# Optimization experiments

Hardware: AMD Instinct MI355X
Metric: run time of the kernel (lower is better)

## Reference

```python
import jax, jax.numpy as jnp
import numpy as np

B, S, D_MODEL = 8, 1024, 1024
N_HEADS, N_KV_HEADS, HEAD_DIM = 16, 8, 64
ROPE_THETA = 10000.0
LN_EPS = 1e-12


def setup_inputs() -> dict:
    key = jax.random.key(0)
    ks = jax.random.split(key, 6)
    sc = 0.02
    return {
        "hidden_states": jax.random.normal(ks[0], (B, S, D_MODEL), jnp.float32),
        "Wq": jax.random.normal(ks[1], (D_MODEL, N_HEADS * HEAD_DIM), jnp.float32) * sc,
        "bq": jnp.zeros((N_HEADS * HEAD_DIM,), jnp.float32),
        "Wk": jax.random.normal(ks[2], (D_MODEL, N_KV_HEADS * HEAD_DIM), jnp.float32) * sc,
        "bk": jnp.zeros((N_KV_HEADS * HEAD_DIM,), jnp.float32),
        "Wv": jax.random.normal(ks[3], (D_MODEL, N_KV_HEADS * HEAD_DIM), jnp.float32) * sc,
        "bv": jnp.zeros((N_KV_HEADS * HEAD_DIM,), jnp.float32),
        "Wo": jax.random.normal(ks[4], (N_HEADS * HEAD_DIM, D_MODEL), jnp.float32) * sc,
        "bo": jnp.zeros((D_MODEL,), jnp.float32),
        "ln_gamma": jnp.ones((D_MODEL,), jnp.float32),
        "ln_beta": jnp.zeros((D_MODEL,), jnp.float32),
    }


def _rope_tables(seq_len, dim, dtype):
    # lucidrains RotaryEmbedding: inv_freq over even indices, interleaved pairs
    inv_freq = 1.0 / (ROPE_THETA ** (jnp.arange(0, dim, 2, dtype=jnp.float32) / dim))
    angles = jnp.arange(seq_len, dtype=jnp.float32)[:, None] * inv_freq[None, :]  # [S, dim/2]
    return jnp.cos(angles).astype(dtype), jnp.sin(angles).astype(dtype)


def _apply_rope(x, cos, sin):
    # x: [B, S, H, D]; rotate interleaved pairs (x0,x1),(x2,x3),...
    x1 = x[..., 0::2]
    x2 = x[..., 1::2]
    c = cos[None, :, None, :]
    s = sin[None, :, None, :]
    y1 = x1 * c - x2 * s
    y2 = x1 * s + x2 * c
    return jnp.stack([y1, y2], axis=-1).reshape(x.shape)


def reference(hidden_states, Wq, bq, Wk, bk, Wv, bv, Wo, bo, ln_gamma, ln_beta):
    b, s, _ = hidden_states.shape
    q = (hidden_states @ Wq + bq).reshape(b, s, N_HEADS, HEAD_DIM)
    k = (hidden_states @ Wk + bk).reshape(b, s, N_KV_HEADS, HEAD_DIM)
    v = (hidden_states @ Wv + bv).reshape(b, s, N_KV_HEADS, HEAD_DIM)

    cos, sin = _rope_tables(s, HEAD_DIM, hidden_states.dtype)
    q = _apply_rope(q, cos, sin)
    k = _apply_rope(k, cos, sin)

    # GQA: repeat_interleave kv heads to match query heads (factor 2)
    rep = N_HEADS // N_KV_HEADS
    k = jnp.repeat(k, rep, axis=2)  # [B, S, H, D]
    v = jnp.repeat(v, rep, axis=2)

    scale = 1.0 / jnp.sqrt(jnp.asarray(HEAD_DIM, hidden_states.dtype))
    scores = jnp.einsum('bqhd,bkhd->bhqk', q * scale, k)  # [B, H, S, S]
    probs = jax.nn.softmax(scores, axis=-1)
    attn = jnp.einsum('bhqk,bkhd->bqhd', probs, v).reshape(b, s, N_HEADS * HEAD_DIM)

    out = attn @ Wo + bo
    resid = out + hidden_states
    mu = jnp.mean(resid, axis=-1, keepdims=True)
    var = jnp.mean(jnp.square(resid - mu), axis=-1, keepdims=True)
    normed = (resid - mu) * jax.lax.rsqrt(var + LN_EPS)
    return normed * ln_gamma + ln_beta
```

## Files before the change

kernel.cpp:

```cpp
#include <hip/hip_runtime.h>
#include <math.h>
#include <stdint.h>

typedef unsigned short u16;
typedef __bf16 bf16x8 __attribute__((ext_vector_type(8)));
typedef float f32x4 __attribute__((ext_vector_type(4)));

typedef const __attribute__((address_space(1))) void gv_t;
typedef __attribute__((address_space(3))) void lv_t;

__device__ __forceinline__ u16 f2bf(float f) {
    unsigned u = __builtin_bit_cast(unsigned, f);
    return (u16)((u + 0x7FFFu + ((u >> 16) & 1u)) >> 16);
}
__device__ __forceinline__ float bf2f(u16 h) {
    return __builtin_bit_cast(float, (unsigned)h << 16);
}
__device__ __forceinline__ void gll16(const void* g, void* l) {
    __builtin_amdgcn_global_load_lds((gv_t*)(uintptr_t)g,
                                     (lv_t*)(unsigned)(uintptr_t)l, 16, 0, 0);
}

__global__ __launch_bounds__(256) void cvt_bf16_kernel(
    const float* __restrict__ in, u16* __restrict__ out, int n4)
{
    int i = blockIdx.x * 256 + threadIdx.x;
    if (i >= n4) return;
    float4 f = ((const float4*)in)[i];
    ushort4 o = make_ushort4(f2bf(f.x), f2bf(f.y), f2bf(f.z), f2bf(f.w));
    ((ushort4*)out)[i] = o;
}

__global__ __launch_bounds__(256) void cvt_t4_kernel(
    const float* __restrict__ w0, const float* __restrict__ w1,
    const float* __restrict__ w2, const float* __restrict__ w3,
    u16* __restrict__ o0, u16* __restrict__ o1,
    u16* __restrict__ o2, u16* __restrict__ o3)
{
    __shared__ u16 t[64][65];
    const float* in; u16* out; int N;
    switch (blockIdx.z) {
        case 0: in = w0; out = o0; N = 1024; break;
        case 1: in = w1; out = o1; N = 512;  break;
        case 2: in = w2; out = o2; N = 512;  break;
        default: in = w3; out = o3; N = 1024; break;
    }
    int kb = blockIdx.y * 64, nb = blockIdx.x * 64;
    if (nb >= N) return;
    int tid = threadIdx.x;
#pragma unroll
    for (int c = 0; c < 16; ++c) {
        int id = c * 256 + tid;
        int r = id >> 6, n = id & 63;
        t[n][r] = f2bf(in[(size_t)(kb + r) * N + nb + n]);
    }
    __syncthreads();
#pragma unroll
    for (int c = 0; c < 16; ++c) {
        int id = c * 256 + tid;
        int r = id >> 6, n = id & 63;
        out[(size_t)(nb + r) * 1024 + kb + n] = t[r][n];
    }
}

template<int MODE>
__global__ __launch_bounds__(256) void gemm_mfma(
    const u16* __restrict__ A, const u16* __restrict__ Bt,
    const float* __restrict__ b0, const float* __restrict__ b1,
    const float* __restrict__ b2,
    const float* __restrict__ resid, float* __restrict__ Cf,
    u16* __restrict__ Qo, u16* __restrict__ Ko, u16* __restrict__ Vto,
    int N, int K)
{
    __shared__ __align__(16) u16 Asl[128 * 64];
    __shared__ __align__(16) u16 Bsl[128 * 64];
    const int tid = threadIdx.x, lane = tid & 63, w = tid >> 6;
    const int quad = lane >> 4, l16 = lane & 15;
    const int bm = blockIdx.y * 128, bn = blockIdx.x * 128;
    const int wm = (w >> 1) * 64, wn = (w & 1) * 64;

    f32x4 acc[4][4] = {};

    const int dr = lane >> 3;
    const int dcs = (((lane & 7) ^ dr) << 3);
    const u16* Ag = &A[(size_t)(bm + w * 32 + dr) * K + dcs];
    const u16* Bg = &Bt[(size_t)(bn + w * 32 + dr) * K + dcs];
    u16* Al = &Asl[(w * 32) * 64];
    u16* Bl = &Bsl[(w * 32) * 64];

    const int sw = l16 & 7;

    for (int k0 = 0; k0 < K; k0 += 64) {
#pragma unroll
        for (int c = 0; c < 4; ++c) {
            gll16(Ag + (size_t)(c * 8) * K + k0, Al + c * 8 * 64);
            gll16(Bg + (size_t)(c * 8) * K + k0, Bl + c * 8 * 64);
        }
        __syncthreads();
        bf16x8 af[4][2], bfr[4][2];
#pragma unroll
        for (int i = 0; i < 4; ++i)
#pragma unroll
            for (int ks = 0; ks < 2; ++ks)
                af[i][ks] = *(const bf16x8*)&Asl[(wm + i * 16 + l16) * 64 + (((ks * 4 + quad) ^ sw) << 3)];
#pragma unroll
        for (int j = 0; j < 4; ++j)
#pragma unroll
            for (int ks = 0; ks < 2; ++ks)
                bfr[j][ks] = *(const bf16x8*)&Bsl[(wn + j * 16 + l16) * 64 + (((ks * 4 + quad) ^ sw) << 3)];
#pragma unroll
        for (int i = 0; i < 4; ++i)
#pragma unroll
            for (int j = 0; j < 4; ++j)
#pragma unroll
                for (int ks = 0; ks < 2; ++ks)
                    acc[i][j] = __builtin_amdgcn_mfma_f32_16x16x32_bf16(af[i][ks], bfr[j][ks], acc[i][j], 0, 0, 0);
        __syncthreads();
    }

#pragma unroll
    for (int j = 0; j < 4; ++j) {
        int col = bn + wn + j * 16 + l16;
        if (MODE == 1) {
            float bb = b0[col];
#pragma unroll
            for (int i = 0; i < 4; ++i) {
                int row0 = bm + wm + i * 16 + quad * 4;
#pragma unroll
                for (int r = 0; r < 4; ++r) {
                    size_t off = (size_t)(row0 + r) * N + col;
                    Cf[off] = acc[i][j][r] + bb + resid[off];
                }
            }
        } else if (col < 1024) {
            float bb = b0[col];
#pragma unroll
            for (int i = 0; i < 4; ++i) {
                int row0 = bm + wm + i * 16 + quad * 4;
#pragma unroll
                for (int r = 0; r < 4; ++r)
                    Qo[(size_t)(row0 + r) * 1024 + col] = f2bf(acc[i][j][r] + bb);
            }
        } else if (col < 1536) {
            int c2 = col - 1024;
            float bb = b1[c2];
#pragma unroll
            for (int i = 0; i < 4; ++i) {
                int row0 = bm + wm + i * 16 + quad * 4;
#pragma unroll
                for (int r = 0; r < 4; ++r)
                    Ko[(size_t)(row0 + r) * 512 + c2] = f2bf(acc[i][j][r] + bb);
            }
        } else {
            int c2 = col - 1536, kvh = c2 >> 6, d = c2 & 63;
            float bb = b2[c2];
#pragma unroll
            for (int i = 0; i < 4; ++i) {
                int row0 = bm + wm + i * 16 + quad * 4;
                int b = row0 >> 10, s = row0 & 1023;
                ushort4 o4;
                o4.x = f2bf(acc[i][j][0] + bb);
                o4.y = f2bf(acc[i][j][1] + bb);
                o4.z = f2bf(acc[i][j][2] + bb);
                o4.w = f2bf(acc[i][j][3] + bb);
                *(ushort4*)&Vto[(size_t)((b * 8 + kvh) * 64 + d) * 1024 + s] = o4;
            }
        }
    }
}

__global__ __launch_bounds__(256) void rope_bf16_kernel(
    u16* __restrict__ x, int shift, int stride, int total)
{
    int idx = blockIdx.x * 256 + threadIdx.x;
    if (idx >= total) return;
    int j = idx & 31;
    int h = (idx >> 5) & ((1 << shift) - 1);
    int row = idx >> (5 + shift);
    int pos = row & 1023;
    float inv = exp2f((float)j * -0.4152410118609203f);
    float sn, cs;
    sincosf((float)pos * inv, &sn, &cs);
    unsigned* p = (unsigned*)&x[(size_t)row * stride + h * 64 + (j << 1)];
    unsigned u = *p;
    float x1 = bf2f((u16)(u & 0xffff)), x2 = bf2f((u16)(u >> 16));
    float y1 = x1 * cs - x2 * sn, y2 = x1 * sn + x2 * cs;
    *p = (unsigned)f2bf(y1) | ((unsigned)f2bf(y2) << 16);
}

__global__ __launch_bounds__(256) void attn_mfma(
    const u16* __restrict__ Q, const u16* __restrict__ K,
    const u16* __restrict__ Vt, u16* __restrict__ O)
{
    __shared__ __align__(16) u16 Ks[64 * 64];
    __shared__ __align__(16) u16 Vts[64 * 64];
    __shared__ __align__(16) u16 Ps[128][40];

    const int tid = threadIdx.x, lane = tid & 63, w = tid >> 6;
    const int quad = lane >> 4, l16 = lane & 15;
    const int qt = blockIdx.x, h = blockIdx.y, b = blockIdx.z;
    const int kvh = h >> 1;
    const size_t qrow0 = (size_t)b * 1024 + qt * 128;
    const size_t krow0 = (size_t)b * 1024;
    const u16* Vg = Vt + (size_t)((b * 8 + kvh) * 64) * 1024;

    const int dr = lane >> 3;
    const int dcs = (((lane & 7) ^ dr) << 3);
    const u16* Kg0 = &K[(krow0 + w * 16 + dr) * 512 + kvh * 64 + dcs];
    const u16* Vg0 = &Vg[(size_t)(w * 16 + dr) * 1024 + dcs];
    u16* Kl0 = &Ks[(w * 16) * 64];
    u16* Vl0 = &Vts[(w * 16) * 64];
    const int sw = l16 & 7;

    bf16x8 qf[2][2];
#pragma unroll
    for (int qg = 0; qg < 2; ++qg) {
        int qrow = w * 32 + qg * 16 + l16;
        float fpos = (float)(qt * 128 + qrow);
#pragma unroll
        for (int ks = 0; ks < 2; ++ks) {
            uint4 qraw = *(const uint4*)&Q[(qrow0 + qrow) * 1024 + h * 64 + ks * 32 + quad * 8];
            unsigned o_[4];
#pragma unroll
            for (int t = 0; t < 4; ++t) {
                int j = ks * 16 + quad * 4 + t;
                float inv = exp2f((float)j * -0.4152410118609203f);
                float sn_, cs_;
                sincosf(fpos * inv, &sn_, &cs_);
                unsigned u = (&qraw.x)[t];
                float x1 = bf2f((u16)(u & 0xffff)), x2 = bf2f((u16)(u >> 16));
                float y1 = x1 * cs_ - x2 * sn_, y2 = x1 * sn_ + x2 * cs_;
                o_[t] = (unsigned)f2bf(y1) | ((unsigned)f2bf(y2) << 16);
            }
            qf[qg][ks] = __builtin_bit_cast(bf16x8, make_uint4(o_[0], o_[1], o_[2], o_[3]));
        }
    }

    f32x4 acc_o[2][4] = {};
    float l_i[2] = {0.f, 0.f};
    const float C1 = 0.18033688011112043f;

    for (int kt = 0; kt < 16; ++kt) {
#pragma unroll
        for (int c = 0; c < 2; ++c) {
            gll16(Kg0 + (size_t)(kt * 64 + c * 8) * 512, Kl0 + c * 8 * 64);
            gll16(Vg0 + (size_t)(c * 8) * 1024 + kt * 64, Vl0 + c * 8 * 64);
        }
        __syncthreads();

        f32x4 s[2][4] = {};
#pragma unroll
        for (int ks = 0; ks < 2; ++ks) {
#pragma unroll
            for (int nt = 0; nt < 4; ++nt) {
                bf16x8 ak = *(const bf16x8*)&Ks[(nt * 16 + l16) * 64 + (((ks * 4 + quad) ^ sw) << 3)];
                s[0][nt] = __builtin_amdgcn_mfma_f32_16x16x32_bf16(ak, qf[0][ks], s[0][nt], 0, 0, 0);
                s[1][nt] = __builtin_amdgcn_mfma_f32_16x16x32_bf16(ak, qf[1][ks], s[1][nt], 0, 0, 0);
            }
        }

#pragma unroll
        for (int kc = 0; kc < 2; ++kc) {
#pragma unroll
            for (int qg = 0; qg < 2; ++qg) {
                float sum = 0.f;
#pragma unroll
                for (int ntl = 0; ntl < 2; ++ntl) {
                    int nt = kc * 2 + ntl;
                    unsigned pk0, pk1;
                    {
                        float p0 = __builtin_amdgcn_exp2f(s[qg][nt][0] * C1);
                        float p1 = __builtin_amdgcn_exp2f(s[qg][nt][1] * C1);
                        unsigned u0 = __builtin_bit_cast(unsigned, p0);
                        unsigned u1 = __builtin_bit_cast(unsigned, p1);
                        sum += __builtin_bit_cast(float, u0 & 0xffff0000u);
                        sum += __builtin_bit_cast(float, u1 & 0xffff0000u);
                        pk0 = __builtin_amdgcn_perm(u1, u0, 0x07060302u);
                    }
                    {
                        float p0 = __builtin_amdgcn_exp2f(s[qg][nt][2] * C1);
                        float p1 = __builtin_amdgcn_exp2f(s[qg][nt][3] * C1);
                        unsigned u0 = __builtin_bit_cast(unsigned, p0);
                        unsigned u1 = __builtin_bit_cast(unsigned, p1);
                        sum += __builtin_bit_cast(float, u0 & 0xffff0000u);
                        sum += __builtin_bit_cast(float, u1 & 0xffff0000u);
                        pk1 = __builtin_amdgcn_perm(u1, u0, 0x07060302u);
                    }
                    *(uint2*)&Ps[w * 32 + qg * 16 + l16][ntl * 16 + quad * 4] = make_uint2(pk0, pk1);
                }
                l_i[qg] += sum;
            }
            bf16x8 bp0 = *(const bf16x8*)&Ps[w * 32 + l16][quad * 8];
            bf16x8 bp1 = *(const bf16x8*)&Ps[w * 32 + 16 + l16][quad * 8];
#pragma unroll
            for (int nt = 0; nt < 4; ++nt) {
                bf16x8 av = *(const bf16x8*)&Vts[(nt * 16 + l16) * 64 + (((kc * 4 + quad) ^ sw) << 3)];
                acc_o[0][nt] = __builtin_amdgcn_mfma_f32_16x16x32_bf16(av, bp0, acc_o[0][nt], 0, 0, 0);
                acc_o[1][nt] = __builtin_amdgcn_mfma_f32_16x16x32_bf16(av, bp1, acc_o[1][nt], 0, 0, 0);
            }
        }
        __syncthreads();
    }

#pragma unroll
    for (int qg = 0; qg < 2; ++qg) {
        float li = l_i[qg];
        li += __shfl_xor(li, 16);
        li += __shfl_xor(li, 32);
        float rl = 1.0f / li;
        size_t orow = (qrow0 + w * 32 + qg * 16 + l16) * 1024 + h * 64;
#pragma unroll
        for (int nt = 0; nt < 4; ++nt) {
            ushort4 o4;
            o4.x = f2bf(acc_o[qg][nt][0] * rl);
            o4.y = f2bf(acc_o[qg][nt][1] * rl);
            o4.z = f2bf(acc_o[qg][nt][2] * rl);
            o4.w = f2bf(acc_o[qg][nt][3] * rl);
            *(ushort4*)&O[orow + nt * 16 + quad * 4] = o4;
        }
    }
}

__global__ __launch_bounds__(256) void ln_kernel(float* __restrict__ io,
    const float* __restrict__ gamma, const float* __restrict__ beta)
{
    int row = blockIdx.x;
    int tid = threadIdx.x;
    float* p = io + (size_t)row * 1024;
    float4 x = *reinterpret_cast<const float4*>(&p[tid << 2]);
    float s = x.x + x.y + x.z + x.w;
    float ss = fmaf(x.x, x.x, fmaf(x.y, x.y, fmaf(x.z, x.z, x.w * x.w)));
#pragma unroll
    for (int off = 32; off > 0; off >>= 1) {
        s  += __shfl_down(s, off);
        ss += __shfl_down(ss, off);
    }
    __shared__ float rs[4], rss[4];
    int lane = tid & 63, wid = tid >> 6;
    if (lane == 0) { rs[wid] = s; rss[wid] = ss; }
    __syncthreads();
    float S = rs[0] + rs[1] + rs[2] + rs[3];
    float SS = rss[0] + rss[1] + rss[2] + rss[3];
    float mu = S * (1.0f / 1024.0f);
    float var = SS * (1.0f / 1024.0f) - mu * mu;
    float rstd = rsqrtf(var + 1e-12f);
    float4 g = *reinterpret_cast<const float4*>(&gamma[tid << 2]);
    float4 be = *reinterpret_cast<const float4*>(&beta[tid << 2]);
    float4 o;
    o.x = (x.x - mu) * rstd * g.x + be.x;
    o.y = (x.y - mu) * rstd * g.y + be.y;
    o.z = (x.z - mu) * rstd * g.z + be.z;
    o.w = (x.w - mu) * rstd * g.w + be.w;
    *reinterpret_cast<float4*>(&p[tid << 2]) = o;
}

extern "C" void kernel_launch(void* const* d_in, const int* in_sizes, int n_in,
                              void* d_out, int out_size, void* d_ws, size_t ws_size,
                              hipStream_t stream)
{
    (void)in_sizes; (void)n_in; (void)out_size; (void)ws_size;
    const float* hidden = (const float*)d_in[0];
    const float* Wq = (const float*)d_in[1];
    const float* bq = (const float*)d_in[2];
    const float* Wk = (const float*)d_in[3];
    const float* bk = (const float*)d_in[4];
    const float* Wv = (const float*)d_in[5];
    const float* bv = (const float*)d_in[6];
    const float* Wo = (const float*)d_in[7];
    const float* bo = (const float*)d_in[8];
    const float* g  = (const float*)d_in[9];
    const float* be = (const float*)d_in[10];
    float* out = (float*)d_out;

    u16* hb  = (u16*)d_ws;
    u16* Wqt = hb  + (size_t)8192 * 1024;
    u16* Wkt = Wqt + (size_t)1024 * 1024;
    u16* Wvt = Wkt + (size_t)512 * 1024;
    u16* Wot = Wvt + (size_t)512 * 1024;
    u16* Qb  = Wot + (size_t)1024 * 1024;
    u16* Kb  = Qb  + (size_t)8192 * 1024;
    u16* Vtb = Kb  + (size_t)8192 * 512;

    cvt_bf16_kernel<<<8192, 256, 0, stream>>>(hidden, hb, 8192 * 1024 / 4);
    cvt_t4_kernel<<<dim3(16, 16, 4), 256, 0, stream>>>(Wq, Wk, Wv, Wo, Wqt, Wkt, Wvt, Wot);

    gemm_mfma<0><<<dim3(16, 64), 256, 0, stream>>>(hb, Wqt, bq, bk, bv,
        nullptr, nullptr, Qb, Kb, Vtb, 2048, 1024);

    rope_bf16_kernel<<<8192, 256, 0, stream>>>(Kb, 3, 512, 8192 * 8 * 32);

    attn_mfma<<<dim3(8, 16, 8), 256, 0, stream>>>(Qb, Kb, Vtb, Qb);

    gemm_mfma<1><<<dim3(8, 64), 256, 0, stream>>>(Qb, Wot, bo, nullptr, nullptr,
        hidden, out, nullptr, nullptr, nullptr, 1024, 1024);
    ln_kernel<<<8192, 256, 0, stream>>>(out, g, be);
}
```

Measured before the change: 269.6 us.

## Double-buffer K/V tiles, fold softmax scale into Q, compute row sums via MFMA

The attention kernel now double-buffers its K and V shared-memory tiles. The next tile's global-to-LDS loads are issued right after the barrier, so they overlap with the current tile's MFMAs, and one of the two barriers per iteration is removed. The softmax scale constant is folded into the RoPE cos/sin applied to Q, which removes a multiply per score. The per-row probability sums are now produced by an extra MFMA against a ones vector instead of scalar adds plus cross-lane shuffles. The cost is twice the K/V LDS footprint, which may lower occupancy, and the single-barrier schedule relies on the next iteration's barrier to prevent write-after-read hazards.

```diff
diff --git a/kernel.cpp b/kernel.cpp
--- a/kernel.cpp
+++ b/kernel.cpp
@@ -192,8 +192,8 @@
     const u16* __restrict__ Q, const u16* __restrict__ K,
     const u16* __restrict__ Vt, u16* __restrict__ O)
 {
-    __shared__ __align__(16) u16 Ks[64 * 64];
-    __shared__ __align__(16) u16 Vts[64 * 64];
+    __shared__ __align__(16) u16 Ks[2][64 * 64];
+    __shared__ __align__(16) u16 Vts[2][64 * 64];
     __shared__ __align__(16) u16 Ps[128][40];
 
     const int tid = threadIdx.x, lane = tid & 63, w = tid >> 6;
@@ -208,9 +208,14 @@
     const int dcs = (((lane & 7) ^ dr) << 3);
     const u16* Kg0 = &K[(krow0 + w * 16 + dr) * 512 + kvh * 64 + dcs];
     const u16* Vg0 = &Vg[(size_t)(w * 16 + dr) * 1024 + dcs];
-    u16* Kl0 = &Ks[(w * 16) * 64];
-    u16* Vl0 = &Vts[(w * 16) * 64];
     const int sw = l16 & 7;
+    const float C1 = 0.18033688011112043f;
+
+#pragma unroll
+    for (int c = 0; c < 2; ++c) {
+        gll16(Kg0 + (size_t)(c * 8) * 512, &Ks[0][(w * 16 + c * 8) * 64]);
+        gll16(Vg0 + (size_t)(c * 8) * 1024, &Vts[0][(w * 16 + c * 8) * 64]);
+    }
 
     bf16x8 qf[2][2];
 #pragma unroll
@@ -227,6 +232,7 @@
                 float inv = exp2f((float)j * -0.4152410118609203f);
                 float sn_, cs_;
                 sincosf(fpos * inv, &sn_, &cs_);
+                cs_ *= C1; sn_ *= C1;
                 unsigned u = (&qraw.x)[t];
                 float x1 = bf2f((u16)(u & 0xffff)), x2 = bf2f((u16)(u >> 16));
                 float y1 = x1 * cs_ - x2 * sn_, y2 = x1 * sn_ + x2 * cs_;
@@ -237,23 +243,30 @@
     }
 
     f32x4 acc_o[2][4] = {};
-    float l_i[2] = {0.f, 0.f};
-    const float C1 = 0.18033688011112043f;
+    f32x4 lsum[2] = {};
+    const bf16x8 ones = __builtin_bit_cast(bf16x8,
+        make_uint4(0x3F803F80u, 0x3F803F80u, 0x3F803F80u, 0x3F803F80u));
 
     for (int kt = 0; kt < 16; ++kt) {
-#pragma unroll
-        for (int c = 0; c < 2; ++c) {
-            gll16(Kg0 + (size_t)(kt * 64 + c * 8) * 512, Kl0 + c * 8 * 64);
-            gll16(Vg0 + (size_t)(c * 8) * 1024 + kt * 64, Vl0 + c * 8 * 64);
-        }
+        const int cur = kt & 1;
         __syncthreads();
 
+        if (kt < 15) {
+#pragma unroll
+            for (int c = 0; c < 2; ++c) {
+                gll16(Kg0 + (size_t)((kt + 1) * 64 + c * 8) * 512,
+                      &Ks[cur ^ 1][(w * 16 + c * 8) * 64]);
+                gll16(Vg0 + (size_t)(c * 8) * 1024 + (kt + 1) * 64,
+                      &Vts[cur ^ 1][(w * 16 + c * 8) * 64]);
+            }
+        }
+
         f32x4 s[2][4] = {};
 #pragma unroll
         for (int ks = 0; ks < 2; ++ks) {
 #pragma unroll
             for (int nt = 0; nt < 4; ++nt) {
-                bf16x8 ak = *(const bf16x8*)&Ks[(nt * 16 + l16) * 64 + (((ks * 4 + quad) ^ sw) << 3)];
+                bf16x8 ak = *(const bf16x8*)&Ks[cur][(nt * 16 + l16) * 64 + (((ks * 4 + quad) ^ sw) << 3)];
                 s[0][nt] = __builtin_amdgcn_mfma_f32_16x16x32_bf16(ak, qf[0][ks], s[0][nt], 0, 0, 0);
                 s[1][nt] = __builtin_amdgcn_mfma_f32_16x16x32_bf16(ak, qf[1][ks], s[1][nt], 0, 0, 0);
             }
@@ -263,51 +276,38 @@
         for (int kc = 0; kc < 2; ++kc) {
 #pragma unroll
             for (int qg = 0; qg < 2; ++qg) {
-                float sum = 0.f;
 #pragma unroll
                 for (int ntl = 0; ntl < 2; ++ntl) {
                     int nt = kc * 2 + ntl;
-                    unsigned pk0, pk1;
-                    {
-                        float p0 = __builtin_amdgcn_exp2f(s[qg][nt][0] * C1);
-                        float p1 = __builtin_amdgcn_exp2f(s[qg][nt][1] * C1);
-                        unsigned u0 = __builtin_bit_cast(unsigned, p0);
-                        unsigned u1 = __builtin_bit_cast(unsigned, p1);
-                        sum += __builtin_bit_cast(float, u0 & 0xffff0000u);
-                        sum += __builtin_bit_cast(float, u1 & 0xffff0000u);
-                        pk0 = __builtin_amdgcn_perm(u1, u0, 0x07060302u);
-                    }
-                    {
-                        float p0 = __builtin_amdgcn_exp2f(s[qg][nt][2] * C1);
-                        float p1 = __builtin_amdgcn_exp2f(s[qg][nt][3] * C1);
-                        unsigned u0 = __builtin_bit_cast(unsigned, p0);
-                        unsigned u1 = __builtin_bit_cast(unsigned, p1);
-                        sum += __builtin_bit_cast(float, u0 & 0xffff0000u);
-                        sum += __builtin_bit_cast(float, u1 & 0xffff0000u);
-                        pk1 = __builtin_amdgcn_perm(u1, u0, 0x07060302u);
-                    }
+                    float p0 = __builtin_amdgcn_exp2f(s[qg][nt][0]);
+                    float p1 = __builtin_amdgcn_exp2f(s[qg][nt][1]);
+                    unsigned pk0 = __builtin_amdgcn_perm(
+                        __builtin_bit_cast(unsigned, p1),
+                        __builtin_bit_cast(unsigned, p0), 0x07060302u);
+                    float p2 = __builtin_amdgcn_exp2f(s[qg][nt][2]);
+                    float p3 = __builtin_amdgcn_exp2f(s[qg][nt][3]);
+                    unsigned pk1 = __builtin_amdgcn_perm(
+                        __builtin_bit_cast(unsigned, p3),
+                        __builtin_bit_cast(unsigned, p2), 0x07060302u);
                     *(uint2*)&Ps[w * 32 + qg * 16 + l16][ntl * 16 + quad * 4] = make_uint2(pk0, pk1);
                 }
-                l_i[qg] += sum;
             }
             bf16x8 bp0 = *(const bf16x8*)&Ps[w * 32 + l16][quad * 8];
             bf16x8 bp1 = *(const bf16x8*)&Ps[w * 32 + 16 + l16][quad * 8];
+            lsum[0] = __builtin_amdgcn_mfma_f32_16x16x32_bf16(ones, bp0, lsum[0], 0, 0, 0);
+            lsum[1] = __builtin_amdgcn_mfma_f32_16x16x32_bf16(ones, bp1, lsum[1], 0, 0, 0);
 #pragma unroll
             for (int nt = 0; nt < 4; ++nt) {
-                bf16x8 av = *(const bf16x8*)&Vts[(nt * 16 + l16) * 64 + (((kc * 4 + quad) ^ sw) << 3)];
+                bf16x8 av = *(const bf16x8*)&Vts[cur][(nt * 16 + l16) * 64 + (((kc * 4 + quad) ^ sw) << 3)];
                 acc_o[0][nt] = __builtin_amdgcn_mfma_f32_16x16x32_bf16(av, bp0, acc_o[0][nt], 0, 0, 0);
                 acc_o[1][nt] = __builtin_amdgcn_mfma_f32_16x16x32_bf16(av, bp1, acc_o[1][nt], 0, 0, 0);
             }
         }
-        __syncthreads();
     }
 
 #pragma unroll
     for (int qg = 0; qg < 2; ++qg) {
-        float li = l_i[qg];
-        li += __shfl_xor(li, 16);
-        li += __shfl_xor(li, 32);
-        float rl = 1.0f / li;
+        float rl = 1.0f / lsum[qg][0];
         size_t orow = (qrow0 + w * 32 + qg * 16 + l16) * 1024 + h * 64;
 #pragma unroll
         for (int nt = 0; nt < 4; ++nt) {
```

Result: faster. 261.0 us (-3.2%).
